# Performance work log

Measured on AMD Instinct MI355X. Metric: run time of the kernel, lower is better.

The kernel has to match this reference:

```python
import jax, jax.numpy as jnp
import numpy as np

N, E, G = 65536, 262144, 2048
DIN, H, F, L, P, TASK = 9, 300, 32, 5, 3, 1
DG = H + F + 1024 + 167  # 1523


def setup_inputs() -> dict:
    key = jax.random.key(0)
    ks = jax.random.split(key, 24)
    s = 0.02
    inp = {
        'x': jax.random.normal(ks[0], (N, DIN), jnp.float32),
        'morgan': jax.random.uniform(ks[1], (G, 1024), jnp.float32),
        'maccs': jax.random.uniform(ks[2], (G, 167), jnp.float32),
        'edge_index': jax.random.randint(ks[3], (2, E), 0, N, jnp.int32),
        'batch': jnp.sort(jax.random.randint(ks[4], (N,), 0, G, jnp.int32)),
        # node feature encoder
        'W_emb': s * jax.random.normal(ks[5], (DIN, H), jnp.float32),
        'b_emb': jnp.zeros((H,), jnp.float32),
        # GIN conv MLPs (L layers): H -> 2H -> H
        'gin_W1': s * jax.random.normal(ks[6], (L, H, 2 * H), jnp.float32),
        'gin_b1': jnp.zeros((L, 2 * H), jnp.float32),
        'gin_W2': s * jax.random.normal(ks[7], (L, 2 * H, H), jnp.float32),
        'gin_b2': jnp.zeros((L, H), jnp.float32),
        'bn_scale': jnp.ones((L, H), jnp.float32),
        'bn_bias': jnp.zeros((L, H), jnp.float32),
        'eps': jnp.zeros((L,), jnp.float32),
        # virtual node: init embedding + update MLPs (L-1 layers)
        'vn0': jnp.zeros((H,), jnp.float32),
        'vn_W1': s * jax.random.normal(ks[8], (L - 1, H, 2 * H), jnp.float32),
        'vn_b1': jnp.zeros((L - 1, 2 * H), jnp.float32),
        'vn_W2': s * jax.random.normal(ks[9], (L - 1, 2 * H, H), jnp.float32),
        'vn_b2': jnp.zeros((L - 1, H), jnp.float32),
        # predictor MLP: DG -> 2H -> TASK
        'Wp1': s * jax.random.normal(ks[10], (DG, 2 * H), jnp.float32),
        'bp1': jnp.zeros((2 * H,), jnp.float32),
        'Wp2': s * jax.random.normal(ks[11], (2 * H, TASK), jnp.float32),
        'bp2': jnp.zeros((TASK,), jnp.float32),
    }
    return inp


def _seg_mean(v, seg, n):
    s = jax.ops.segment_sum(v, seg, num_segments=n)
    c = jax.ops.segment_sum(jnp.ones((v.shape[0], 1), v.dtype), seg, num_segments=n)
    return s / jnp.maximum(c, 1.0)


def _bn(z, scale, bias):
    m = z.mean(0)
    v = z.var(0)
    return (z - m) * jax.lax.rsqrt(v + 1e-5) * scale + bias


def _gnn_and_predict(x, morgan, maccs, W_emb, b_emb, gin_W1, gin_b1, gin_W2, gin_b2,
                     bn_scale, bn_bias, eps, vn0, vn_W1, vn_b1, vn_W2, vn_b2,
                     Wp1, bp1, Wp2, bp2, edge_index, batch):
    n = x.shape[0]
    g = morgan.shape[0]
    nl = gin_W1.shape[0]
    src, dst = edge_index[0], edge_index[1]

    # GIN-virtual backbone (eval mode, dropout off). Note: GNN input is the
    # original x (the permuted ids are appended AFTER the GNN), so h is
    # permutation-independent and computed once.
    h = x @ W_emb + b_emb
    vn = jnp.broadcast_to(vn0, (g, vn0.shape[0]))
    for l in range(nl):
        hv = h + vn[batch]                                       # [N,H]
        agg = jax.ops.segment_sum(hv[src], dst, num_segments=n)  # neighbor sum
        z = (1.0 + eps[l]) * hv + agg
        z = jax.nn.relu(z @ gin_W1[l] + gin_b1[l]) @ gin_W2[l] + gin_b2[l]
        z = _bn(z, bn_scale[l], bn_bias[l])
        if l < nl - 1:
            z = jax.nn.relu(z)
        h = h + z  # residual
        if l < nl - 1:  # virtual node update
            vt = jax.ops.segment_sum(hv, batch, num_segments=g) + vn
            vn = vn + jax.nn.relu(jax.nn.relu(vt @ vn_W1[l] + vn_b1[l]) @ vn_W2[l] + vn_b2[l])

    pooled_h = _seg_mean(h, batch, g)  # [G,H]

    # Segmented random permutation of tiled eye(F) ids, averaged over P perms.
    # Each node gets one_hot(perm_rank_within_graph % F); rank computed by a
    # single lexsort over (batch, random) instead of a per-graph Python loop.
    counts = jax.ops.segment_sum(jnp.ones((n,), jnp.int32), batch, num_segments=g)
    starts = jnp.concatenate([jnp.zeros((1,), jnp.int32),
                              jnp.cumsum(counts)[:-1].astype(jnp.int32)])
    pkey = jax.random.key(42)
    acc = jnp.zeros((g, F), h.dtype)
    for p in range(P):
        r = jax.random.uniform(jax.random.fold_in(pkey, p), (n,))
        order = jnp.lexsort((r, batch))                       # sort by graph, then random
        local = jnp.arange(n, dtype=jnp.int32) - starts[batch[order]]
        rank = jnp.zeros((n,), jnp.int32).at[order].set(local)  # random rank in graph
        ids = jax.nn.one_hot(rank % F, F, dtype=h.dtype)        # [N,F]
        acc = acc + _seg_mean(ids, batch, g)
    id_pool = acc / P

    # h_rep order matches torch: [pooled h | pooled ids | morgan | maccs]
    h_rep = jnp.concatenate([pooled_h, id_pool, morgan, maccs], axis=1)  # [G,1523]
    return jax.nn.relu(h_rep @ Wp1 + bp1) @ Wp2 + bp2  # [G,TASK]


def reference(x, morgan, maccs, W_emb, b_emb, gin_W1, gin_b1, gin_W2, gin_b2,
              bn_scale, bn_bias, eps, vn0, vn_W1, vn_b1, vn_W2, vn_b2,
              Wp1, bp1, Wp2, bp2, edge_index, batch):
    return _gnn_and_predict(x, morgan, maccs, W_emb, b_emb, gin_W1, gin_b1,
                            gin_W2, gin_b2, bn_scale, bn_bias, eps, vn0,
                            vn_W1, vn_b1, vn_W2, vn_b2, Wp1, bp1, Wp2, bp2,
                            edge_index, batch)
```

## Files before the change

### kernel.cpp

```cpp
#include <hip/hip_runtime.h>

typedef unsigned short u16;
typedef unsigned int u32;
typedef __attribute__((ext_vector_type(8))) short bf16x8_t;
typedef __attribute__((ext_vector_type(4))) float f32x4_t;

#define kN 65536
#define kE 262144
#define kG 2048
#define kH 300
#define kH2 600
#define kL 5
#define kF 32
#define kDG 1523
#define KP_H 320
#define KP_H2 640
#define KP_DG 1536
#define NP_H2 640
#define NP_H 320
#define HVS 320
#define HVS32 160
#define WFRAG_PER_L 204800

__device__ __forceinline__ float bf2f(u16 x) {
    union { u32 u; float f; } v; v.u = ((u32)x) << 16; return v.f;
}
__device__ __forceinline__ u16 f2bf(float f) {
    union { float f; u32 u; } v; v.f = f;
    u32 u = v.u;
    u32 r = (u + 0x7fffu + ((u >> 16) & 1u)) >> 16;
    return (u16)r;
}
__device__ __forceinline__ float blo(u32 v) { return bf2f((u16)(v & 0xffffu)); }
__device__ __forceinline__ float bhi(u32 v) { return bf2f((u16)(v >> 16)); }
__device__ __forceinline__ u32 pack2(float lo, float hi) {
    return (u32)f2bf(lo) | ((u32)f2bf(hi) << 16);
}

__device__ __forceinline__ void gld16(const u16* g, u16* l) {
    __builtin_amdgcn_global_load_lds(
        (const __attribute__((address_space(1))) u32*)g,
        (__attribute__((address_space(3))) u32*)l, 16, 0, 0);
}

__device__ __forceinline__ void vwait6() { asm volatile("s_waitcnt vmcnt(6)" ::: "memory"); }
__device__ __forceinline__ void vwait8() { asm volatile("s_waitcnt vmcnt(8)" ::: "memory"); }
__device__ __forceinline__ void vwait0() { asm volatile("s_waitcnt vmcnt(0)" ::: "memory"); }
__device__ __forceinline__ void lwait0() { asm volatile("s_waitcnt lgkmcnt(0)" ::: "memory"); }
__device__ __forceinline__ void rbar() {
    __builtin_amdgcn_sched_barrier(0);
    __builtin_amdgcn_s_barrier();
    __builtin_amdgcn_sched_barrier(0);
}

__device__ __forceinline__ void swz_tile(int& m, int& n) {
    int p = blockIdx.x + gridDim.x * blockIdx.y;
    int xcd = p & 7;
    int q = p >> 3;
    int NB = gridDim.y;
    int mb8 = gridDim.x >> 3;
    m = xcd * mb8 + q / NB;
    n = q % NB;
}

__global__ void transpose_k(const float* __restrict__ W, u16* __restrict__ Wt,
                            int K, int NN, int NP, int KP, long total) {
    long idx = (long)blockIdx.x * 256 + threadIdx.x;
    if (idx >= total) return;
    int per = NP * KP;
    int b = (int)(idx / per);
    int r = (int)(idx % per);
    int n = r / KP;
    int k = r % KP;
    u16 v = 0;
    if (n < NN && k < K) v = f2bf(W[(long)b * K * NN + (long)k * NN + n]);
    Wt[idx] = v;
}

__global__ void pack_w1_k(const float* __restrict__ W, u16* __restrict__ Wf, long total) {
    long idx = (long)blockIdx.x * 256 + threadIdx.x;
    if (idx >= total) return;
    int l = (int)(idx / WFRAG_PER_L);
    long r = idx % WFRAG_PER_L;
    int e = (int)(r & 7);
    long r1 = r >> 3;
    int ln = (int)(r1 & 63);
    int l16 = ln & 15, quad = ln >> 4;
    long s = r1 >> 6;
    int tk = (int)(s % 10);
    long s2 = s / 10;
    int nt = (int)(s2 & 1);
    long s3 = s2 >> 1;
    int w = (int)(s3 & 3);
    int c = (int)(s3 >> 2);
    int n = c * 128 + w * 32 + nt * 16 + l16;
    int k = tk * 32 + quad * 8 + e;
    u16 v = 0;
    if (n < kH2 && k < kH) v = f2bf(W[(long)l * kH * kH2 + (long)k * kH2 + n]);
    Wf[idx] = v;
}

__global__ void pack_w2_k(const float* __restrict__ W, u16* __restrict__ Wf, long total) {
    long idx = (long)blockIdx.x * 256 + threadIdx.x;
    if (idx >= total) return;
    int l = (int)(idx / WFRAG_PER_L);
    long r = idx % WFRAG_PER_L;
    int e = (int)(r & 7);
    long r1 = r >> 3;
    int ln = (int)(r1 & 63);
    int l16 = ln & 15, quad = ln >> 4;
    long s = r1 >> 6;
    int ks = (int)(s & 3);
    long s2 = s >> 2;
    int nt = (int)(s2 % 5);
    long s3 = s2 / 5;
    int w = (int)(s3 & 3);
    int c = (int)(s3 >> 2);
    int n = w * 80 + nt * 16 + l16;
    int k = c * 128 + ks * 32 + quad * 8 + e;
    u16 v = 0;
    if (n < kH && k < kH2) v = f2bf(W[(long)l * kH2 * kH + (long)k * kH + n]);
    Wf[idx] = v;
}

__global__ void hist_g_k(const int* __restrict__ batch, int* __restrict__ counts) {
    int n = blockIdx.x * 256 + threadIdx.x;
    if (n < kN) atomicAdd(&counts[batch[n]], 1);
}

__global__ void scan_g_k(const int* __restrict__ counts, int* __restrict__ starts) {
    __shared__ int s[1024];
    int t = threadIdx.x;
    int c0 = counts[2 * t], c1 = counts[2 * t + 1];
    s[t] = c0 + c1;
    __syncthreads();
    for (int off = 1; off < 1024; off <<= 1) {
        int v = (t >= off) ? s[t - off] : 0;
        __syncthreads();
        s[t] += v;
        __syncthreads();
    }
    int excl = (t > 0) ? s[t - 1] : 0;
    starts[2 * t] = excl;
    starts[2 * t + 1] = excl + c0;
}

__global__ void hist_n_k(const int* __restrict__ ei, int* __restrict__ cnt) {
    int e = blockIdx.x * 256 + threadIdx.x;
    if (e < kE) atomicAdd(&cnt[ei[kE + e]], 1);
}

__global__ void scanA_k(const int* __restrict__ cnt, int* __restrict__ start, int* __restrict__ bsum) {
    __shared__ int s[1024];
    int b = blockIdx.x, t = threadIdx.x;
    int v = cnt[b * 1024 + t];
    s[t] = v;
    __syncthreads();
    for (int off = 1; off < 1024; off <<= 1) {
        int u = (t >= off) ? s[t - off] : 0;
        __syncthreads();
        s[t] += u;
        __syncthreads();
    }
    start[b * 1024 + t] = s[t] - v;
    if (t == 1023) bsum[b] = s[1023];
}

__global__ void scanB_k(int* __restrict__ bsum) {
    if (threadIdx.x == 0) {
        int s = 0;
        for (int i = 0; i < kN / 1024; i++) { s += bsum[i]; bsum[i] = s; }
    }
}

__global__ void scanC_k(int* __restrict__ start, const int* __restrict__ bsum) {
    int b = blockIdx.x, t = threadIdx.x;
    int add = (b > 0) ? bsum[b - 1] : 0;
    start[b * 1024 + t] += add;
    if (b == kN / 1024 - 1 && t == 1023) start[kN] = bsum[kN / 1024 - 1];
}

__global__ void fill_n_k(const int* __restrict__ ei, const int* __restrict__ start,
                         int* __restrict__ fill, int* __restrict__ perm) {
    int e = blockIdx.x * 256 + threadIdx.x;
    if (e >= kE) return;
    int s = ei[e], d = ei[kE + e];
    int pos = start[d] + atomicAdd(&fill[d], 1);
    perm[pos] = s;
}

__global__ __launch_bounds__(256) void embed_k(
    const float* __restrict__ x, const float* __restrict__ W,
    const float* __restrict__ b, const float* __restrict__ vn0,
    u32* __restrict__ hv32) {
    __shared__ float sW[9 * kH];
    __shared__ float sBV[kH];
    int tid = threadIdx.x;
    for (int i = tid; i < 9 * kH; i += 256) sW[i] = W[i];
    for (int i = tid; i < kH; i += 256) sBV[i] = b[i] + vn0[i];
    __syncthreads();
    int wave = tid >> 6, lane = tid & 63;
    int n = blockIdx.x * 4 + wave;
    float xv[9];
    #pragma unroll
    for (int d = 0; d < 9; d++) xv[d] = x[n * 9 + d];
    #pragma unroll
    for (int p = 0; p < 3; p++) {
        int ii = lane + p * 64;
        if (ii < 150) {
            int c0 = 2 * ii;
            float a0 = sBV[c0], a1 = sBV[c0 + 1];
            #pragma unroll
            for (int d = 0; d < 9; d++) {
                a0 += xv[d] * sW[d * kH + c0];
                a1 += xv[d] * sW[d * kH + c0 + 1];
            }
            hv32[(long)n * HVS32 + ii] = pack2(a0, a1);
        } else if (ii < HVS32) {
            hv32[(long)n * HVS32 + ii] = 0u;
        }
    }
}

__global__ void vninit_k(const float* __restrict__ vn0, float* __restrict__ vn) {
    int g = blockIdx.x, c = threadIdx.x;
    if (c < kH) vn[g * kH + c] = vn0[c];
}

__global__ __launch_bounds__(256) void gather_combine_k(
    const u32* __restrict__ hv32, const int* __restrict__ start_n,
    const int* __restrict__ perm, const float* __restrict__ eps, int l,
    u32* __restrict__ out32, float* __restrict__ stats) {
    int tid = threadIdx.x;
    int wave = tid >> 6, lane = tid & 63;
    int n = blockIdx.x * 4 + wave;
    int st = start_n[n], en = start_n[n + 1];
    int i0 = lane, i1 = lane + 64, i2 = lane + 128;
    bool p2 = (i2 < 150);
    float a0 = 0.f, b0 = 0.f, a1 = 0.f, b1 = 0.f, a2 = 0.f, b2 = 0.f;
    int e = st;
    for (; e + 4 <= en; e += 4) {
        const u32* rA = hv32 + (long)perm[e] * HVS32;
        const u32* rB = hv32 + (long)perm[e + 1] * HVS32;
        const u32* rC = hv32 + (long)perm[e + 2] * HVS32;
        const u32* rD = hv32 + (long)perm[e + 3] * HVS32;
        u32 vA0 = rA[i0], vA1 = rA[i1], vA2 = p2 ? rA[i2] : 0u;
        u32 vB0 = rB[i0], vB1 = rB[i1], vB2 = p2 ? rB[i2] : 0u;
        u32 vC0 = rC[i0], vC1 = rC[i1], vC2 = p2 ? rC[i2] : 0u;
        u32 vD0 = rD[i0], vD1 = rD[i1], vD2 = p2 ? rD[i2] : 0u;
        a0 += (blo(vA0) + blo(vB0)) + (blo(vC0) + blo(vD0));
        b0 += (bhi(vA0) + bhi(vB0)) + (bhi(vC0) + bhi(vD0));
        a1 += (blo(vA1) + blo(vB1)) + (blo(vC1) + blo(vD1));
        b1 += (bhi(vA1) + bhi(vB1)) + (bhi(vC1) + bhi(vD1));
        a2 += (blo(vA2) + blo(vB2)) + (blo(vC2) + blo(vD2));
        b2 += (bhi(vA2) + bhi(vB2)) + (bhi(vC2) + bhi(vD2));
    }
    for (; e + 2 <= en; e += 2) {
        const u32* rA = hv32 + (long)perm[e] * HVS32;
        const u32* rB = hv32 + (long)perm[e + 1] * HVS32;
        u32 vA0 = rA[i0], vA1 = rA[i1], vA2 = p2 ? rA[i2] : 0u;
        u32 vB0 = rB[i0], vB1 = rB[i1], vB2 = p2 ? rB[i2] : 0u;
        a0 += blo(vA0) + blo(vB0); b0 += bhi(vA0) + bhi(vB0);
        a1 += blo(vA1) + blo(vB1); b1 += bhi(vA1) + bhi(vB1);
        a2 += blo(vA2) + blo(vB2); b2 += bhi(vA2) + bhi(vB2);
    }
    if (e < en) {
        const u32* rA = hv32 + (long)perm[e] * HVS32;
        u32 vA0 = rA[i0], vA1 = rA[i1], vA2 = p2 ? rA[i2] : 0u;
        a0 += blo(vA0); b0 += bhi(vA0);
        a1 += blo(vA1); b1 += bhi(vA1);
        a2 += blo(vA2); b2 += bhi(vA2);
    }
    const u32* self = hv32 + (long)n * HVS32;
    float ep = 1.f + eps[l];
    u32 s0 = self[i0], s1 = self[i1];
    u32* o = out32 + (long)n * HVS32;
    o[i0] = pack2(ep * blo(s0) + a0, ep * bhi(s0) + b0);
    o[i1] = pack2(ep * blo(s1) + a1, ep * bhi(s1) + b1);
    if (p2) {
        u32 s2 = self[i2];
        o[i2] = pack2(ep * blo(s2) + a2, ep * bhi(s2) + b2);
    } else if (i2 < HVS32) {
        o[i2] = 0u;
    }
    int gz = blockIdx.x * 256 + tid;
    if (gz < 2 * kH) stats[gz] = 0.f;
}

__global__ __launch_bounds__(256) void vt_fin_k(
    const u32* __restrict__ hv32, const float* __restrict__ vncur,
    const int* __restrict__ counts, const int* __restrict__ starts,
    u32* __restrict__ vt32) {
    int tid = threadIdx.x, wave = tid >> 6, lane = tid & 63;
    int g = blockIdx.x * 4 + wave;
    int cnt = counts[g], st = starts[g];
    int i0 = lane, i1 = lane + 64, i2 = lane + 128;
    bool p2 = (i2 < 150);
    float a0 = 0.f, b0 = 0.f, a1 = 0.f, b1 = 0.f, a2 = 0.f, b2 = 0.f;
    int i = 0;
    for (; i + 4 <= cnt; i += 4) {
        const u32* rA = hv32 + (long)(st + i) * HVS32;
        const u32* rB = hv32 + (long)(st + i + 1) * HVS32;
        const u32* rC = hv32 + (long)(st + i + 2) * HVS32;
        const u32* rD = hv32 + (long)(st + i + 3) * HVS32;
        u32 vA0 = rA[i0], vA1 = rA[i1], vA2 = p2 ? rA[i2] : 0u;
        u32 vB0 = rB[i0], vB1 = rB[i1], vB2 = p2 ? rB[i2] : 0u;
        u32 vC0 = rC[i0], vC1 = rC[i1], vC2 = p2 ? rC[i2] : 0u;
        u32 vD0 = rD[i0], vD1 = rD[i1], vD2 = p2 ? rD[i2] : 0u;
        a0 += (blo(vA0) + blo(vB0)) + (blo(vC0) + blo(vD0));
        b0 += (bhi(vA0) + bhi(vB0)) + (bhi(vC0) + bhi(vD0));
        a1 += (blo(vA1) + blo(vB1)) + (blo(vC1) + blo(vD1));
        b1 += (bhi(vA1) + bhi(vB1)) + (bhi(vC1) + bhi(vD1));
        a2 += (blo(vA2) + blo(vB2)) + (blo(vC2) + blo(vD2));
        b2 += (bhi(vA2) + bhi(vB2)) + (bhi(vC2) + bhi(vD2));
    }
    for (; i < cnt; i++) {
        const u32* rA = hv32 + (long)(st + i) * HVS32;
        u32 vA0 = rA[i0], vA1 = rA[i1], vA2 = p2 ? rA[i2] : 0u;
        a0 += blo(vA0); b0 += bhi(vA0);
        a1 += blo(vA1); b1 += bhi(vA1);
        a2 += blo(vA2); b2 += bhi(vA2);
    }
    const float* vg = vncur + g * kH;
    vt32[(long)g * HVS32 + i0] = pack2(a0 + vg[2 * i0], b0 + vg[2 * i0 + 1]);
    vt32[(long)g * HVS32 + i1] = pack2(a1 + vg[2 * i1], b1 + vg[2 * i1 + 1]);
    if (p2) vt32[(long)g * HVS32 + i2] = pack2(a2 + vg[2 * i2], b2 + vg[2 * i2 + 1]);
    else if (i2 < HVS32) vt32[(long)g * HVS32 + i2] = 0u;
}

__global__ __launch_bounds__(256, 2) void fused_mlp_k(
    const u16* __restrict__ A,
    const u16* __restrict__ W1f,
    const float* __restrict__ b1,
    const u16* __restrict__ W2f,
    const float* __restrict__ b2,
    u16* __restrict__ outp,
    float* __restrict__ stats) {
    __shared__ __align__(16) u16 lA[5][64 * 64];
    __shared__ __align__(16) u16 z1c[2][64 * 128];
    __shared__ float sred[320][2];

    const int tid = threadIdx.x;
    const int lane = tid & 63;
    const int wave = tid >> 6;
    const int l16 = lane & 15;
    const int quad = lane >> 4;
    const long tm = (long)blockIdx.x * 64;
    const int srow = lane >> 3;
    const int sch = (lane & 7) ^ srow;

    for (int i = tid; i < 320; i += 256) { sred[i][0] = 0.f; sred[i][1] = 0.f; }

    #pragma unroll
    for (int t = 0; t < 5; t++) {
        #pragma unroll
        for (int j = 0; j < 2; j++) {
            int rb = wave * 16 + j * 8;
            gld16(A + (tm + rb + srow) * KP_H + t * 64 + sch * 8, &lA[t][rb * 64]);
        }
    }

    float rb1[5][2];
    #pragma unroll
    for (int c = 0; c < 5; c++)
        #pragma unroll
        for (int nt = 0; nt < 2; nt++) {
            int gc = c * 128 + wave * 32 + nt * 16 + l16;
            rb1[c][nt] = (gc < kH2) ? b1[gc] : 0.f;
        }
    float rb2[5];
    #pragma unroll
    for (int nt = 0; nt < 5; nt++) {
        int col = wave * 80 + nt * 16 + l16;
        rb2[nt] = (col < kH) ? b2[col] : 0.f;
    }

    f32x4_t acc2[4][5];
    #pragma unroll
    for (int i = 0; i < 4; i++)
        #pragma unroll
        for (int j = 0; j < 5; j++) acc2[i][j] = (f32x4_t){0.f, 0.f, 0.f, 0.f};

    vwait0();
    rbar();

    #pragma unroll
    for (int c = 0; c < 5; c++) {
        f32x4_t acc1[4][2];
        #pragma unroll
        for (int i = 0; i < 4; i++) {
            acc1[i][0] = (f32x4_t){0.f, 0.f, 0.f, 0.f};
            acc1[i][1] = (f32x4_t){0.f, 0.f, 0.f, 0.f};
        }
        const u16* w1p = W1f + ((long)((c * 4 + wave) * 2) * 10) * 512 + lane * 8;
        bf16x8_t wf[4][2];
        #pragma unroll
        for (int p = 0; p < 3; p++) {
            wf[p][0] = *(const bf16x8_t*)(w1p + p * 512);
            wf[p][1] = *(const bf16x8_t*)(w1p + 10 * 512 + p * 512);
        }
        #pragma unroll
        for (int tk = 0; tk < 10; tk++) {
            if (tk + 3 < 10) {
                wf[(tk + 3) & 3][0] = *(const bf16x8_t*)(w1p + (tk + 3) * 512);
                wf[(tk + 3) & 3][1] = *(const bf16x8_t*)(w1p + 10 * 512 + (tk + 3) * 512);
            }
            const int t = tk >> 1, ks = tk & 1;
            bf16x8_t af[4];
            #pragma unroll
            for (int mt = 0; mt < 4; mt++) {
                int row = mt * 16 + l16;
                int phys = (ks * 4 + quad) ^ (l16 & 7);
                af[mt] = *(const bf16x8_t*)&lA[t][row * 64 + phys * 8];
            }
            __builtin_amdgcn_s_setprio(1);
            #pragma unroll
            for (int mt = 0; mt < 4; mt++) {
                acc1[mt][0] = __builtin_amdgcn_mfma_f32_16x16x32_bf16(af[mt], wf[tk & 3][0], acc1[mt][0], 0, 0, 0);
                acc1[mt][1] = __builtin_amdgcn_mfma_f32_16x16x32_bf16(af[mt], wf[tk & 3][1], acc1[mt][1], 0, 0, 0);
            }
            __builtin_amdgcn_s_setprio(0);
        }

        const u16* w2p = W2f + ((long)((c * 4 + wave) * 5) * 4) * 512 + lane * 8;
        bf16x8_t wg[2][5];
        #pragma unroll
        for (int nt = 0; nt < 5; nt++) {
            wg[0][nt] = *(const bf16x8_t*)(w2p + nt * 4 * 512);
            wg[1][nt] = *(const bf16x8_t*)(w2p + nt * 4 * 512 + 512);
        }

        u16* zb = z1c[c & 1];
        #pragma unroll
        for (int nt = 0; nt < 2; nt++) {
            int col = wave * 32 + nt * 16 + l16;
            #pragma unroll
            for (int mt = 0; mt < 4; mt++) {
                #pragma unroll
                for (int r = 0; r < 4; r++) {
                    int row = mt * 16 + quad * 4 + r;
                    float v = fmaxf(acc1[mt][nt][r] + rb1[c][nt], 0.f);
                    int phys = (col >> 3) ^ (row & 15);
                    zb[row * 128 + phys * 8 + (col & 7)] = f2bf(v);
                }
            }
        }
        lwait0();
        rbar();

        #pragma unroll
        for (int ks = 0; ks < 4; ks++) {
            bf16x8_t af[4];
            #pragma unroll
            for (int mt = 0; mt < 4; mt++) {
                int row = mt * 16 + l16;
                int phys = (ks * 4 + quad) ^ (row & 15);
                af[mt] = *(const bf16x8_t*)&zb[row * 128 + phys * 8];
            }
            __builtin_amdgcn_s_setprio(1);
            #pragma unroll
            for (int mt = 0; mt < 4; mt++)
                #pragma unroll
                for (int nt = 0; nt < 5; nt++)
                    acc2[mt][nt] = __builtin_amdgcn_mfma_f32_16x16x32_bf16(af[mt], wg[ks & 1][nt], acc2[mt][nt], 0, 0, 0);
            __builtin_amdgcn_s_setprio(0);
            if (ks + 2 < 4) {
                #pragma unroll
                for (int nt = 0; nt < 5; nt++)
                    wg[ks & 1][nt] = *(const bf16x8_t*)(w2p + nt * 4 * 512 + (ks + 2) * 512);
            }
        }
    }

    #pragma unroll
    for (int nt = 0; nt < 5; nt++) {
        int col = wave * 80 + nt * 16 + l16;
        float s = 0.f, s2 = 0.f;
        #pragma unroll
        for (int mt = 0; mt < 4; mt++) {
            #pragma unroll
            for (int r = 0; r < 4; r++) {
                long row = tm + mt * 16 + quad * 4 + r;
                float v = acc2[mt][nt][r] + rb2[nt];
                float sv = (col < kH) ? v : 0.f;
                outp[row * KP_H + col] = f2bf(sv);
                s += sv; s2 += sv * sv;
            }
        }
        atomicAdd(&sred[col][0], s);
        atomicAdd(&sred[col][1], s2);
    }
    __syncthreads();
    for (int i = tid; i < kH; i += 256) {
        atomicAdd(&stats[i], sred[i][0]);
        atomicAdd(&stats[kH + i], sred[i][1]);
    }
}

template<int ACT, int OUT_BF16, int BN_STATS>
__global__ __launch_bounds__(256) void gemm_k(
    const u16* __restrict__ A, const u16* __restrict__ Wt,
    const float* __restrict__ bias, void* __restrict__ out,
    float* __restrict__ stats,
    int KP, int NN, int out_stride, int store_cols) {
    __shared__ __align__(16) u16 lA[2][128 * 64];
    __shared__ __align__(16) u16 lB[2][128 * 64];
    __shared__ float sred[128][2];

    const int tid = threadIdx.x;
    const int lane = tid & 63;
    const int wave = tid >> 6;
    const int l16 = lane & 15;
    const int quad = lane >> 4;
    const int wm = (wave & 1) * 64;
    const int wn = (wave >> 1) * 64;
    int sm, sn;
    swz_tile(sm, sn);
    const long tm = (long)sm * 128;
    const int tn = sn * 128;

    const int srow = lane >> 3;
    const int sch = (lane & 7) ^ srow;

    f32x4_t acc[4][4];
    #pragma unroll
    for (int i = 0; i < 4; i++)
        #pragma unroll
        for (int j = 0; j < 4; j++) acc[i][j] = (f32x4_t){0.f, 0.f, 0.f, 0.f};

    auto stage = [&](int bb, int k0) {
        #pragma unroll
        for (int j = 0; j < 4; j++) {
            int rb = wave * 32 + j * 8;
            int r = rb + srow;
            gld16(A + (tm + r) * KP + k0 + sch * 8, &lA[bb][rb * 64]);
            gld16(Wt + (long)(tn + r) * KP + k0 + sch * 8, &lB[bb][rb * 64]);
        }
    };

    const int nk = KP >> 6;
    stage(0, 0);
    if (nk > 1) stage(1, 64);
    for (int t = 0; t < nk; t++) {
        if (t < nk - 1) vwait8(); else vwait0();
        rbar();
        const u16* la = lA[t & 1];
        const u16* lb = lB[t & 1];
        #pragma unroll
        for (int ks = 0; ks < 2; ks++) {
            bf16x8_t af[4], bfr[4];
            #pragma unroll
            for (int mt = 0; mt < 4; mt++) {
                int row = wm + mt * 16 + l16;
                int phys = (ks * 4 + quad) ^ (l16 & 7);
                af[mt] = *(const bf16x8_t*)&la[row * 64 + phys * 8];
            }
            #pragma unroll
            for (int nt = 0; nt < 4; nt++) {
                int row = wn + nt * 16 + l16;
                int phys = (ks * 4 + quad) ^ (l16 & 7);
                bfr[nt] = *(const bf16x8_t*)&lb[row * 64 + phys * 8];
            }
            #pragma unroll
            for (int mt = 0; mt < 4; mt++)
                #pragma unroll
                for (int nt = 0; nt < 4; nt++)
                    acc[mt][nt] = __builtin_amdgcn_mfma_f32_16x16x32_bf16(af[mt], bfr[nt], acc[mt][nt], 0, 0, 0);
        }
        rbar();
        if (t + 2 < nk) stage(t & 1, (t + 2) * 64);
    }

    if (BN_STATS) {
        if (tid < 128) { sred[tid][0] = 0.f; sred[tid][1] = 0.f; }
    }
    __syncthreads();

    #pragma unroll
    for (int nt = 0; nt < 4; nt++) {
        int col = tn + wn + nt * 16 + l16;
        float bv = (col < NN) ? bias[col] : 0.f;
        float s = 0.f, s2 = 0.f;
        #pragma unroll
        for (int mt = 0; mt < 4; mt++) {
            #pragma unroll
            for (int r = 0; r < 4; r++) {
                long row = tm + wm + mt * 16 + quad * 4 + r;
                float v = acc[mt][nt][r] + bv;
                if (ACT) v = fmaxf(v, 0.f);
                float sv = (col < NN) ? v : 0.f;
                if (col < store_cols) {
                    if (OUT_BF16) ((u16*)out)[row * out_stride + col] = f2bf(sv);
                    else          ((float*)out)[row * out_stride + col] = sv;
                }
                s += sv; s2 += sv * sv;
            }
        }
        if (BN_STATS) {
            atomicAdd(&sred[wn + nt * 16 + l16][0], s);
            atomicAdd(&sred[wn + nt * 16 + l16][1], s2);
        }
    }
    if (BN_STATS) {
        __syncthreads();
        if (tid < 128) {
            int col = tn + tid;
            if (col < NN) {
                atomicAdd(&stats[col], sred[tid][0]);
                atomicAdd(&stats[NN + col], sred[tid][1]);
            }
        }
    }
}

template<int ACT, int OUT_MODE, int BN_STATS>
__global__ __launch_bounds__(256) void gemm64_k(
    const u16* __restrict__ A, const u16* __restrict__ Wt,
    const float* __restrict__ bias, void* __restrict__ out,
    float* __restrict__ stats, const float* __restrict__ vnacc,
    int KP, int NN, int out_stride, int store_cols) {
    __shared__ __align__(16) u16 lA[2][128 * 64];
    __shared__ __align__(16) u16 lB[2][64 * 64];
    __shared__ float sred[64][2];

    const int tid = threadIdx.x;
    const int lane = tid & 63;
    const int wave = tid >> 6;
    const int l16 = lane & 15;
    const int quad = lane >> 4;
    const int wm = (wave & 1) * 64;
    const int wn = (wave >> 1) * 32;
    int sm, sn;
    swz_tile(sm, sn);
    const long tm = (long)sm * 128;
    const int tn = sn * 64;

    const int srow = lane >> 3;
    const int sch = (lane & 7) ^ srow;

    f32x4_t acc[4][2];
    #pragma unroll
    for (int i = 0; i < 4; i++)
        #pragma unroll
        for (int j = 0; j < 2; j++) acc[i][j] = (f32x4_t){0.f, 0.f, 0.f, 0.f};

    auto stage = [&](int bb, int k0) {
        #pragma unroll
        for (int j = 0; j < 4; j++) {
            int rb = wave * 32 + j * 8;
            gld16(A + (tm + rb + srow) * KP + k0 + sch * 8, &lA[bb][rb * 64]);
        }
        #pragma unroll
        for (int j = 0; j < 2; j++) {
            int rb = wave * 16 + j * 8;
            gld16(Wt + (long)(tn + rb + srow) * KP + k0 + sch * 8, &lB[bb][rb * 64]);
        }
    };

    const int nk = KP >> 6;
    stage(0, 0);
    if (nk > 1) stage(1, 64);
    for (int t = 0; t < nk; t++) {
        if (t < nk - 1) vwait6(); else vwait0();
        rbar();
        const u16* la = lA[t & 1];
        const u16* lb = lB[t & 1];
        #pragma unroll
        for (int ks = 0; ks < 2; ks++) {
            bf16x8_t af[4], bfr[2];
            #pragma unroll
            for (int mt = 0; mt < 4; mt++) {
                int row = wm + mt * 16 + l16;
                int phys = (ks * 4 + quad) ^ (l16 & 7);
                af[mt] = *(const bf16x8_t*)&la[row * 64 + phys * 8];
            }
            #pragma unroll
            for (int nt = 0; nt < 2; nt++) {
                int row = wn + nt * 16 + l16;
                int phys = (ks * 4 + quad) ^ (l16 & 7);
                bfr[nt] = *(const bf16x8_t*)&lb[row * 64 + phys * 8];
            }
            #pragma unroll
            for (int mt = 0; mt < 4; mt++)
                #pragma unroll
                for (int nt = 0; nt < 2; nt++)
                    acc[mt][nt] = __builtin_amdgcn_mfma_f32_16x16x32_bf16(af[mt], bfr[nt], acc[mt][nt], 0, 0, 0);
        }
        rbar();
        if (t + 2 < nk) stage(t & 1, (t + 2) * 64);
    }

    if (BN_STATS) {
        if (tid < 64) { sred[tid][0] = 0.f; sred[tid][1] = 0.f; }
    }
    __syncthreads();

    #pragma unroll
    for (int nt = 0; nt < 2; nt++) {
        int col = tn + wn + nt * 16 + l16;
        float bv = (col < NN) ? bias[col] : 0.f;
        float s = 0.f, s2 = 0.f;
        #pragma unroll
        for (int mt = 0; mt < 4; mt++) {
            #pragma unroll
            for (int r = 0; r < 4; r++) {
                long row = tm + wm + mt * 16 + quad * 4 + r;
                float v = acc[mt][nt][r] + bv;
                if (ACT) v = fmaxf(v, 0.f);
                float sv = (col < NN) ? v : 0.f;
                if (col < store_cols) {
                    if (OUT_MODE == 1) ((u16*)out)[row * out_stride + col] = f2bf(sv);
                    else if (OUT_MODE == 2)
                        ((float*)out)[row * out_stride + col] =
                            vnacc[row * out_stride + col] + fmaxf(v, 0.f);
                    else ((float*)out)[row * out_stride + col] = sv;
                }
                s += sv; s2 += sv * sv;
            }
        }
        if (BN_STATS) {
            atomicAdd(&sred[wn + nt * 16 + l16][0], s);
            atomicAdd(&sred[wn + nt * 16 + l16][1], s2);
        }
    }
    if (BN_STATS) {
        __syncthreads();
        if (tid < 64) {
            int col = tn + tid;
            if (col < NN) {
                atomicAdd(&stats[col], sred[tid][0]);
                atomicAdd(&stats[NN + col], sred[tid][1]);
            }
        }
    }
}

template<int RELU>
__global__ __launch_bounds__(256) void resid_k(
    u32* __restrict__ hvb32, const u32* __restrict__ z32,
    const float* __restrict__ stats,
    const float* __restrict__ scale, const float* __restrict__ bias, int l,
    const int* __restrict__ batch,
    const float* __restrict__ vncur, const float* __restrict__ vnnxt) {
    int tid = threadIdx.x;
    int wave = tid >> 6, lane = tid & 63;
    int n = blockIdx.x * 4 + wave;
    int g = batch[n];
    #pragma unroll
    for (int p = 0; p < 3; p++) {
        int ii = lane + p * 64;
        if (ii >= 150) break;
        int c0 = 2 * ii;
        float m0 = stats[c0] * (1.f / (float)kN), m1 = stats[c0 + 1] * (1.f / (float)kN);
        float v0 = fmaxf(stats[kH + c0] * (1.f / (float)kN) - m0 * m0, 0.f);
        float v1 = fmaxf(stats[kH + c0 + 1] * (1.f / (float)kN) - m1 * m1, 0.f);
        float a0 = scale[l * kH + c0] * rsqrtf(v0 + 1e-5f);
        float a1 = scale[l * kH + c0 + 1] * rsqrtf(v1 + 1e-5f);
        float d0 = bias[l * kH + c0] - m0 * a0;
        float d1 = bias[l * kH + c0 + 1] - m1 * a1;
        u32 zz = z32[(long)n * HVS32 + ii];
        u32 ho = hvb32[(long)n * HVS32 + ii];
        float2 vc = *(const float2*)(vncur + g * kH + c0);
        float2 vx = *(const float2*)(vnnxt + g * kH + c0);
        float t0 = blo(zz) * a0 + d0;
        float t1 = bhi(zz) * a1 + d1;
        if (RELU) { t0 = fmaxf(t0, 0.f); t1 = fmaxf(t1, 0.f); }
        float h0 = (blo(ho) - vc.x) + t0;
        float h1 = (bhi(ho) - vc.y) + t1;
        hvb32[(long)n * HVS32 + ii] = pack2(h0 + vx.x, h1 + vx.y);
    }
}

__global__ __launch_bounds__(256) void pooled_k(
    const u32* __restrict__ hv32, const float* __restrict__ vnlast,
    const int* __restrict__ counts, const int* __restrict__ starts,
    u32* __restrict__ hrep32) {
    int tid = threadIdx.x, wave = tid >> 6, lane = tid & 63;
    int g = blockIdx.x * 4 + wave;
    int cnt = counts[g], st = starts[g];
    int i0 = lane, i1 = lane + 64, i2 = lane + 128;
    bool p2 = (i2 < 150);
    float a0 = 0.f, b0 = 0.f, a1 = 0.f, b1 = 0.f, a2 = 0.f, b2 = 0.f;
    int i = 0;
    for (; i + 4 <= cnt; i += 4) {
        const u32* rA = hv32 + (long)(st + i) * HVS32;
        const u32* rB = hv32 + (long)(st + i + 1) * HVS32;
        const u32* rC = hv32 + (long)(st + i + 2) * HVS32;
        const u32* rD = hv32 + (long)(st + i + 3) * HVS32;
        u32 vA0 = rA[i0], vA1 = rA[i1], vA2 = p2 ? rA[i2] : 0u;
        u32 vB0 = rB[i0], vB1 = rB[i1], vB2 = p2 ? rB[i2] : 0u;
        u32 vC0 = rC[i0], vC1 = rC[i1], vC2 = p2 ? rC[i2] : 0u;
        u32 vD0 = rD[i0], vD1 = rD[i1], vD2 = p2 ? rD[i2] : 0u;
        a0 += (blo(vA0) + blo(vB0)) + (blo(vC0) + blo(vD0));
        b0 += (bhi(vA0) + bhi(vB0)) + (bhi(vC0) + bhi(vD0));
        a1 += (blo(vA1) + blo(vB1)) + (blo(vC1) + blo(vD1));
        b1 += (bhi(vA1) + bhi(vB1)) + (bhi(vC1) + bhi(vD1));
        a2 += (blo(vA2) + blo(vB2)) + (blo(vC2) + blo(vD2));
        b2 += (bhi(vA2) + bhi(vB2)) + (bhi(vC2) + bhi(vD2));
    }
    for (; i < cnt; i++) {
        const u32* rA = hv32 + (long)(st + i) * HVS32;
        u32 vA0 = rA[i0], vA1 = rA[i1], vA2 = p2 ? rA[i2] : 0u;
        a0 += blo(vA0); b0 += bhi(vA0);
        a1 += blo(vA1); b1 += bhi(vA1);
        a2 += blo(vA2); b2 += bhi(vA2);
    }
    float fc = (float)cnt;
    float inv = 1.f / (float)(cnt > 0 ? cnt : 1);
    const float* vg = vnlast + g * kH;
    hrep32[(long)g * 768 + i0] = pack2((a0 - fc * vg[2 * i0]) * inv, (b0 - fc * vg[2 * i0 + 1]) * inv);
    hrep32[(long)g * 768 + i1] = pack2((a1 - fc * vg[2 * i1]) * inv, (b1 - fc * vg[2 * i1 + 1]) * inv);
    if (p2)
        hrep32[(long)g * 768 + i2] = pack2((a2 - fc * vg[2 * i2]) * inv, (b2 - fc * vg[2 * i2 + 1]) * inv);
}

__global__ void hrep_rest_k(const float* __restrict__ morgan, const float* __restrict__ maccs,
                            const int* __restrict__ counts, u16* __restrict__ hrep) {
    long idx = (long)blockIdx.x * 256 + threadIdx.x;
    if (idx >= (long)kG * (KP_DG - kH)) return;
    int g = (int)(idx / (KP_DG - kH));
    int j = (int)(idx % (KP_DG - kH));
    int col = kH + j;
    u16 v;
    if (j < kF) {
        int c = counts[g];
        int q = (j < c) ? ((c - 1 - j) / kF + 1) : 0;
        v = f2bf((float)q / (float)(c > 0 ? c : 1));
    } else if (j < kF + 1024) {
        v = f2bf(morgan[(long)g * 1024 + (j - kF)]);
    } else if (j < kF + 1024 + 167) {
        v = f2bf(maccs[(long)g * 167 + (j - kF - 1024)]);
    } else {
        v = 0;
    }
    hrep[(long)g * KP_DG + col] = v;
}

__global__ void final_k(const u16* __restrict__ zp, const float* __restrict__ Wp2,
                        const float* __restrict__ bp2, float* __restrict__ out) {
    int wave = threadIdx.x >> 6, lane = threadIdx.x & 63;
    int g = blockIdx.x * 4 + wave;
    float acc = 0.f;
    for (int c = lane; c < kH2; c += 64) acc += bf2f(zp[(long)g * KP_H2 + c]) * Wp2[c];
    #pragma unroll
    for (int off = 32; off; off >>= 1) acc += __shfl_down(acc, off);
    if (lane == 0) out[g] = acc + bp2[0];
}

extern "C" void kernel_launch(void* const* d_in, const int* in_sizes, int n_in,
                              void* d_out, int out_size, void* d_ws, size_t ws_size,
                              hipStream_t stream) {
    const float* x      = (const float*)d_in[0];
    const float* morgan = (const float*)d_in[1];
    const float* maccs  = (const float*)d_in[2];
    const int*   ei     = (const int*)d_in[3];
    const int*   batch  = (const int*)d_in[4];
    const float* W_emb  = (const float*)d_in[5];
    const float* b_emb  = (const float*)d_in[6];
    const float* gin_W1 = (const float*)d_in[7];
    const float* gin_b1 = (const float*)d_in[8];
    const float* gin_W2 = (const float*)d_in[9];
    const float* gin_b2 = (const float*)d_in[10];
    const float* bn_scale = (const float*)d_in[11];
    const float* bn_bias  = (const float*)d_in[12];
    const float* eps    = (const float*)d_in[13];
    const float* vn0    = (const float*)d_in[14];
    const float* vn_W1  = (const float*)d_in[15];
    const float* vn_b1  = (const float*)d_in[16];
    const float* vn_W2  = (const float*)d_in[17];
    const float* vn_b2  = (const float*)d_in[18];
    const float* Wp1    = (const float*)d_in[19];
    const float* bp1    = (const float*)d_in[20];
    const float* Wp2    = (const float*)d_in[21];
    const float* bp2    = (const float*)d_in[22];
    float* out = (float*)d_out;

    char* ws = (char*)d_ws;
    size_t off = 0;
    auto alloc = [&](size_t bytes) -> char* {
        char* p = ws + off;
        off += (bytes + 255) & ~(size_t)255;
        return p;
    };
    u16*   hvbf = (u16*)alloc((size_t)kN * HVS * 2);
    u16*   hv   = (u16*)alloc((size_t)kN * KP_H * 2);
    u16*   z1   = (u16*)alloc((size_t)kN * KP_H2 * 2);
    float* vnA  = (float*)alloc((size_t)kG * kH * 4);
    float* vnB  = (float*)alloc((size_t)kG * kH * 4);
    int* counts = (int*)alloc(kG * 4);
    int* starts = (int*)alloc(kG * 4);
    float* stats = (float*)alloc(2 * kH * 4);
    int* cnt_n  = (int*)alloc((size_t)kN * 4);
    int* start_n = (int*)alloc((size_t)(kN + 1) * 4);
    int* fill_n = (int*)alloc((size_t)kN * 4);
    int* bsum   = (int*)alloc((kN / 1024) * 4);
    int* perm   = (int*)alloc((size_t)kE * 4);
    u16* W1f   = (u16*)alloc((size_t)kL * WFRAG_PER_L * 2);
    u16* W2f   = (u16*)alloc((size_t)kL * WFRAG_PER_L * 2);
    u16* Wt_v1 = (u16*)alloc((size_t)(kL - 1) * NP_H2 * KP_H * 2);
    u16* Wt_v2 = (u16*)alloc((size_t)(kL - 1) * NP_H * KP_H2 * 2);
    u16* Wt_p1 = (u16*)alloc((size_t)NP_H2 * KP_DG * 2);
    if (off > ws_size) return;

    u16* vt_in = z1;
    u16* z1v   = z1 + (size_t)4 * 1024 * 1024;
    u16* hrep  = z1;
    u16* zp    = z1 + (size_t)8 * 1024 * 1024;
    float* vnb[2] = {vnA, vnB};

    {
        long tf = (long)kL * WFRAG_PER_L;
        pack_w1_k<<<dim3((unsigned)((tf + 255) / 256)), 256, 0, stream>>>(gin_W1, W1f, tf);
        pack_w2_k<<<dim3((unsigned)((tf + 255) / 256)), 256, 0, stream>>>(gin_W2, W2f, tf);
        long t3 = (long)(kL - 1) * NP_H2 * KP_H;
        transpose_k<<<dim3((unsigned)((t3 + 255) / 256)), 256, 0, stream>>>(vn_W1, Wt_v1, kH, kH2, NP_H2, KP_H, t3);
        long t4 = (long)(kL - 1) * NP_H * KP_H2;
        transpose_k<<<dim3((unsigned)((t4 + 255) / 256)), 256, 0, stream>>>(vn_W2, Wt_v2, kH2, kH, NP_H, KP_H2, t4);
        long t5 = (long)NP_H2 * KP_DG;
        transpose_k<<<dim3((unsigned)((t5 + 255) / 256)), 256, 0, stream>>>(Wp1, Wt_p1, kDG, kH2, NP_H2, KP_DG, t5);
    }

    hipMemsetAsync(counts, 0, kG * 4, stream);
    hipMemsetAsync(cnt_n, 0, (size_t)kN * 4, stream);
    hipMemsetAsync(fill_n, 0, (size_t)kN * 4, stream);
    hist_g_k<<<kN / 256, 256, 0, stream>>>(batch, counts);
    scan_g_k<<<1, 1024, 0, stream>>>(counts, starts);
    hist_n_k<<<kE / 256, 256, 0, stream>>>(ei, cnt_n);
    scanA_k<<<kN / 1024, 1024, 0, stream>>>(cnt_n, start_n, bsum);
    scanB_k<<<1, 64, 0, stream>>>(bsum);
    scanC_k<<<kN / 1024, 1024, 0, stream>>>(start_n, bsum);
    fill_n_k<<<kE / 256, 256, 0, stream>>>(ei, start_n, fill_n, perm);

    embed_k<<<kN / 4, 256, 0, stream>>>(x, W_emb, b_emb, vn0, (u32*)hvbf);
    vninit_k<<<kG, 320, 0, stream>>>(vn0, vnA);

    for (int l = 0; l < kL; l++) {
        float* vcur = vnb[l & 1];
        float* vnxt = vnb[(l + 1) & 1];
        gather_combine_k<<<kN / 4, 256, 0, stream>>>(
            (const u32*)hvbf, start_n, perm, eps, l, (u32*)hv, stats);
        if (l < kL - 1) {
            vt_fin_k<<<kG / 4, 256, 0, stream>>>(
                (const u32*)hvbf, vcur, counts, starts, (u32*)vt_in);
            gemm_k<1, 1, 0><<<dim3(16, NP_H2 / 128), 256, 0, stream>>>(
                vt_in, Wt_v1 + (size_t)l * NP_H2 * KP_H, vn_b1 + l * kH2,
                z1v, nullptr, KP_H, kH2, KP_H2, KP_H2);
            gemm64_k<0, 2, 0><<<dim3(16, NP_H / 64), 256, 0, stream>>>(
                z1v, Wt_v2 + (size_t)l * NP_H * KP_H2, vn_b2 + l * kH,
                vnxt, nullptr, vcur, KP_H2, kH, kH, kH);
        }
        fused_mlp_k<<<kN / 64, 256, 0, stream>>>(
            hv, W1f + (size_t)l * WFRAG_PER_L, gin_b1 + l * kH2,
            W2f + (size_t)l * WFRAG_PER_L, gin_b2 + l * kH,
            hv, stats);
        if (l < kL - 1)
            resid_k<1><<<kN / 4, 256, 0, stream>>>(
                (u32*)hvbf, (const u32*)hv, stats, bn_scale, bn_bias, l, batch, vcur, vnxt);
        else
            resid_k<0><<<kN / 4, 256, 0, stream>>>(
                (u32*)hvbf, (const u32*)hv, stats, bn_scale, bn_bias, l, batch, vcur, vcur);
    }

    float* vnlast = vnb[(kL - 1) & 1];
    pooled_k<<<kG / 4, 256, 0, stream>>>(
        (const u32*)hvbf, vnlast, counts, starts, (u32*)hrep);
    {
        long tr = (long)kG * (KP_DG - kH);
        hrep_rest_k<<<dim3((unsigned)((tr + 255) / 256)), 256, 0, stream>>>(morgan, maccs, counts, hrep);
    }
    gemm_k<1, 1, 0><<<dim3(16, NP_H2 / 128), 256, 0, stream>>>(
        hrep, Wt_p1, bp1, zp, nullptr, KP_DG, kH2, KP_H2, KP_H2);
    final_k<<<kG / 4, 256, 0, stream>>>(zp, Wp2, bp2, out);
}
```

Before: 1.151 ms.

## Fuse virtual-node two-layer MLP into single kernel with packed weight fragments

Replaces the two separate GEMM launches for the virtual-node MLP (H->2H with ReLU, then 2H->H plus residual) with one fused kernel. The kernel keeps each 64-row block's hidden activations in shared memory and reads pre-packed MFMA weight fragments, the same layout the GIN MLP kernel uses. This removes the global round trip of the 2048x640 intermediate and one launch per layer. In exchange the grid is small: only 32 blocks, each of which streams all weights, so occupancy for this step drops.

Result: no change. 1.128 ms (-1.9%).

```diff
diff --git a/kernel.cpp b/kernel.cpp
--- a/kernel.cpp
+++ b/kernel.cpp
@@ -43,7 +43,6 @@
         (__attribute__((address_space(3))) u32*)l, 16, 0, 0);
 }
 
-__device__ __forceinline__ void vwait6() { asm volatile("s_waitcnt vmcnt(6)" ::: "memory"); }
 __device__ __forceinline__ void vwait8() { asm volatile("s_waitcnt vmcnt(8)" ::: "memory"); }
 __device__ __forceinline__ void vwait0() { asm volatile("s_waitcnt vmcnt(0)" ::: "memory"); }
 __device__ __forceinline__ void lwait0() { asm volatile("s_waitcnt lgkmcnt(0)" ::: "memory"); }
@@ -497,6 +496,164 @@
     }
 }
 
+__global__ __launch_bounds__(256, 2) void fused_vn_k(
+    const u16* __restrict__ A,
+    const u16* __restrict__ W1f,
+    const float* __restrict__ b1,
+    const u16* __restrict__ W2f,
+    const float* __restrict__ b2,
+    const float* __restrict__ vncur,
+    float* __restrict__ vnnxt) {
+    __shared__ __align__(16) u16 lA[5][64 * 64];
+    __shared__ __align__(16) u16 z1c[2][64 * 128];
+
+    const int tid = threadIdx.x;
+    const int lane = tid & 63;
+    const int wave = tid >> 6;
+    const int l16 = lane & 15;
+    const int quad = lane >> 4;
+    const long tm = (long)blockIdx.x * 64;
+    const int srow = lane >> 3;
+    const int sch = (lane & 7) ^ srow;
+
+    #pragma unroll
+    for (int t = 0; t < 5; t++) {
+        #pragma unroll
+        for (int j = 0; j < 2; j++) {
+            int rb = wave * 16 + j * 8;
+            gld16(A + (tm + rb + srow) * KP_H + t * 64 + sch * 8, &lA[t][rb * 64]);
+        }
+    }
+
+    float rb1[5][2];
+    #pragma unroll
+    for (int c = 0; c < 5; c++)
+        #pragma unroll
+        for (int nt = 0; nt < 2; nt++) {
+            int gc = c * 128 + wave * 32 + nt * 16 + l16;
+            rb1[c][nt] = (gc < kH2) ? b1[gc] : 0.f;
+        }
+    float rb2[5];
+    #pragma unroll
+    for (int nt = 0; nt < 5; nt++) {
+        int col = wave * 80 + nt * 16 + l16;
+        rb2[nt] = (col < kH) ? b2[col] : 0.f;
+    }
+
+    f32x4_t acc2[4][5];
+    #pragma unroll
+    for (int i = 0; i < 4; i++)
+        #pragma unroll
+        for (int j = 0; j < 5; j++) acc2[i][j] = (f32x4_t){0.f, 0.f, 0.f, 0.f};
+
+    vwait0();
+    rbar();
+
+    #pragma unroll
+    for (int c = 0; c < 5; c++) {
+        f32x4_t acc1[4][2];
+        #pragma unroll
+        for (int i = 0; i < 4; i++) {
+            acc1[i][0] = (f32x4_t){0.f, 0.f, 0.f, 0.f};
+            acc1[i][1] = (f32x4_t){0.f, 0.f, 0.f, 0.f};
+        }
+        const u16* w1p = W1f + ((long)((c * 4 + wave) * 2) * 10) * 512 + lane * 8;
+        bf16x8_t wf[4][2];
+        #pragma unroll
+        for (int p = 0; p < 3; p++) {
+            wf[p][0] = *(const bf16x8_t*)(w1p + p * 512);
+            wf[p][1] = *(const bf16x8_t*)(w1p + 10 * 512 + p * 512);
+        }
+        #pragma unroll
+        for (int tk = 0; tk < 10; tk++) {
+            if (tk + 3 < 10) {
+                wf[(tk + 3) & 3][0] = *(const bf16x8_t*)(w1p + (tk + 3) * 512);
+                wf[(tk + 3) & 3][1] = *(const bf16x8_t*)(w1p + 10 * 512 + (tk + 3) * 512);
+            }
+            const int t = tk >> 1, ks = tk & 1;
+            bf16x8_t af[4];
+            #pragma unroll
+            for (int mt = 0; mt < 4; mt++) {
+                int row = mt * 16 + l16;
+                int phys = (ks * 4 + quad) ^ (l16 & 7);
+                af[mt] = *(const bf16x8_t*)&lA[t][row * 64 + phys * 8];
+            }
+            __builtin_amdgcn_s_setprio(1);
+            #pragma unroll
+            for (int mt = 0; mt < 4; mt++) {
+                acc1[mt][0] = __builtin_amdgcn_mfma_f32_16x16x32_bf16(af[mt], wf[tk & 3][0], acc1[mt][0], 0, 0, 0);
+                acc1[mt][1] = __builtin_amdgcn_mfma_f32_16x16x32_bf16(af[mt], wf[tk & 3][1], acc1[mt][1], 0, 0, 0);
+            }
+            __builtin_amdgcn_s_setprio(0);
+        }
+
+        const u16* w2p = W2f + ((long)((c * 4 + wave) * 5) * 4) * 512 + lane * 8;
+        bf16x8_t wg[2][5];
+        #pragma unroll
+        for (int nt = 0; nt < 5; nt++) {
+            wg[0][nt] = *(const bf16x8_t*)(w2p + nt * 4 * 512);
+            wg[1][nt] = *(const bf16x8_t*)(w2p + nt * 4 * 512 + 512);
+        }
+
+        u16* zb = z1c[c & 1];
+        #pragma unroll
+        for (int nt = 0; nt < 2; nt++) {
+            int col = wave * 32 + nt * 16 + l16;
+            #pragma unroll
+            for (int mt = 0; mt < 4; mt++) {
+                #pragma unroll
+                for (int r = 0; r < 4; r++) {
+                    int row = mt * 16 + quad * 4 + r;
+                    float v = fmaxf(acc1[mt][nt][r] + rb1[c][nt], 0.f);
+                    int phys = (col >> 3) ^ (row & 15);
+                    zb[row * 128 + phys * 8 + (col & 7)] = f2bf(v);
+                }
+            }
+        }
+        lwait0();
+        rbar();
+
+        #pragma unroll
+        for (int ks = 0; ks < 4; ks++) {
+            bf16x8_t af[4];
+            #pragma unroll
+            for (int mt = 0; mt < 4; mt++) {
+                int row = mt * 16 + l16;
+                int phys = (ks * 4 + quad) ^ (row & 15);
+                af[mt] = *(const bf16x8_t*)&zb[row * 128 + phys * 8];
+            }
+            __builtin_amdgcn_s_setprio(1);
+            #pragma unroll
+            for (int mt = 0; mt < 4; mt++)
+                #pragma unroll
+                for (int nt = 0; nt < 5; nt++)
+                    acc2[mt][nt] = __builtin_amdgcn_mfma_f32_16x16x32_bf16(af[mt], wg[ks & 1][nt], acc2[mt][nt], 0, 0, 0);
+            __builtin_amdgcn_s_setprio(0);
+            if (ks + 2 < 4) {
+                #pragma unroll
+                for (int nt = 0; nt < 5; nt++)
+                    wg[ks & 1][nt] = *(const bf16x8_t*)(w2p + nt * 4 * 512 + (ks + 2) * 512);
+            }
+        }
+    }
+
+    #pragma unroll
+    for (int nt = 0; nt < 5; nt++) {
+        int col = wave * 80 + nt * 16 + l16;
+        if (col < kH) {
+            #pragma unroll
+            for (int mt = 0; mt < 4; mt++) {
+                #pragma unroll
+                for (int r = 0; r < 4; r++) {
+                    long row = tm + mt * 16 + quad * 4 + r;
+                    float v = fmaxf(acc2[mt][nt][r] + rb2[nt], 0.f);
+                    vnnxt[row * kH + col] = vncur[row * kH + col] + v;
+                }
+            }
+        }
+    }
+}
+
 template<int ACT, int OUT_BF16, int BN_STATS>
 __global__ __launch_bounds__(256) void gemm_k(
     const u16* __restrict__ A, const u16* __restrict__ Wt,
@@ -604,128 +761,6 @@
     if (BN_STATS) {
         __syncthreads();
         if (tid < 128) {
-            int col = tn + tid;
-            if (col < NN) {
-                atomicAdd(&stats[col], sred[tid][0]);
-                atomicAdd(&stats[NN + col], sred[tid][1]);
-            }
-        }
-    }
-}
-
-template<int ACT, int OUT_MODE, int BN_STATS>
-__global__ __launch_bounds__(256) void gemm64_k(
-    const u16* __restrict__ A, const u16* __restrict__ Wt,
-    const float* __restrict__ bias, void* __restrict__ out,
-    float* __restrict__ stats, const float* __restrict__ vnacc,
-    int KP, int NN, int out_stride, int store_cols) {
-    __shared__ __align__(16) u16 lA[2][128 * 64];
-    __shared__ __align__(16) u16 lB[2][64 * 64];
-    __shared__ float sred[64][2];
-
-    const int tid = threadIdx.x;
-    const int lane = tid & 63;
-    const int wave = tid >> 6;
-    const int l16 = lane & 15;
-    const int quad = lane >> 4;
-    const int wm = (wave & 1) * 64;
-    const int wn = (wave >> 1) * 32;
-    int sm, sn;
-    swz_tile(sm, sn);
-    const long tm = (long)sm * 128;
-    const int tn = sn * 64;
-
-    const int srow = lane >> 3;
-    const int sch = (lane & 7) ^ srow;
-
-    f32x4_t acc[4][2];
-    #pragma unroll
-    for (int i = 0; i < 4; i++)
-        #pragma unroll
-        for (int j = 0; j < 2; j++) acc[i][j] = (f32x4_t){0.f, 0.f, 0.f, 0.f};
-
-    auto stage = [&](int bb, int k0) {
-        #pragma unroll
-        for (int j = 0; j < 4; j++) {
-            int rb = wave * 32 + j * 8;
-            gld16(A + (tm + rb + srow) * KP + k0 + sch * 8, &lA[bb][rb * 64]);
-        }
-        #pragma unroll
-        for (int j = 0; j < 2; j++) {
-            int rb = wave * 16 + j * 8;
-            gld16(Wt + (long)(tn + rb + srow) * KP + k0 + sch * 8, &lB[bb][rb * 64]);
-        }
-    };
-
-    const int nk = KP >> 6;
-    stage(0, 0);
-    if (nk > 1) stage(1, 64);
-    for (int t = 0; t < nk; t++) {
-        if (t < nk - 1) vwait6(); else vwait0();
-        rbar();
-        const u16* la = lA[t & 1];
-        const u16* lb = lB[t & 1];
-        #pragma unroll
-        for (int ks = 0; ks < 2; ks++) {
-            bf16x8_t af[4], bfr[2];
-            #pragma unroll
-            for (int mt = 0; mt < 4; mt++) {
-                int row = wm + mt * 16 + l16;
-                int phys = (ks * 4 + quad) ^ (l16 & 7);
-                af[mt] = *(const bf16x8_t*)&la[row * 64 + phys * 8];
-            }
-            #pragma unroll
-            for (int nt = 0; nt < 2; nt++) {
-                int row = wn + nt * 16 + l16;
-                int phys = (ks * 4 + quad) ^ (l16 & 7);
-                bfr[nt] = *(const bf16x8_t*)&lb[row * 64 + phys * 8];
-            }
-            #pragma unroll
-            for (int mt = 0; mt < 4; mt++)
-                #pragma unroll
-                for (int nt = 0; nt < 2; nt++)
-                    acc[mt][nt] = __builtin_amdgcn_mfma_f32_16x16x32_bf16(af[mt], bfr[nt], acc[mt][nt], 0, 0, 0);
-        }
-        rbar();
-        if (t + 2 < nk) stage(t & 1, (t + 2) * 64);
-    }
-
-    if (BN_STATS) {
-        if (tid < 64) { sred[tid][0] = 0.f; sred[tid][1] = 0.f; }
-    }
-    __syncthreads();
-
-    #pragma unroll
-    for (int nt = 0; nt < 2; nt++) {
-        int col = tn + wn + nt * 16 + l16;
-        float bv = (col < NN) ? bias[col] : 0.f;
-        float s = 0.f, s2 = 0.f;
-        #pragma unroll
-        for (int mt = 0; mt < 4; mt++) {
-            #pragma unroll
-            for (int r = 0; r < 4; r++) {
-                long row = tm + wm + mt * 16 + quad * 4 + r;
-                float v = acc[mt][nt][r] + bv;
-                if (ACT) v = fmaxf(v, 0.f);
-                float sv = (col < NN) ? v : 0.f;
-                if (col < store_cols) {
-                    if (OUT_MODE == 1) ((u16*)out)[row * out_stride + col] = f2bf(sv);
-                    else if (OUT_MODE == 2)
-                        ((float*)out)[row * out_stride + col] =
-                            vnacc[row * out_stride + col] + fmaxf(v, 0.f);
-                    else ((float*)out)[row * out_stride + col] = sv;
-                }
-                s += sv; s2 += sv * sv;
-            }
-        }
-        if (BN_STATS) {
-            atomicAdd(&sred[wn + nt * 16 + l16][0], s);
-            atomicAdd(&sred[wn + nt * 16 + l16][1], s2);
-        }
-    }
-    if (BN_STATS) {
-        __syncthreads();
-        if (tid < 64) {
             int col = tn + tid;
             if (col < NN) {
                 atomicAdd(&stats[col], sred[tid][0]);
@@ -897,13 +932,12 @@
     int* perm   = (int*)alloc((size_t)kE * 4);
     u16* W1f   = (u16*)alloc((size_t)kL * WFRAG_PER_L * 2);
     u16* W2f   = (u16*)alloc((size_t)kL * WFRAG_PER_L * 2);
-    u16* Wt_v1 = (u16*)alloc((size_t)(kL - 1) * NP_H2 * KP_H * 2);
-    u16* Wt_v2 = (u16*)alloc((size_t)(kL - 1) * NP_H * KP_H2 * 2);
+    u16* Wv1f  = (u16*)alloc((size_t)(kL - 1) * WFRAG_PER_L * 2);
+    u16* Wv2f  = (u16*)alloc((size_t)(kL - 1) * WFRAG_PER_L * 2);
     u16* Wt_p1 = (u16*)alloc((size_t)NP_H2 * KP_DG * 2);
     if (off > ws_size) return;
 
     u16* vt_in = z1;
-    u16* z1v   = z1 + (size_t)4 * 1024 * 1024;
     u16* hrep  = z1;
     u16* zp    = z1 + (size_t)8 * 1024 * 1024;
     float* vnb[2] = {vnA, vnB};
@@ -912,10 +946,9 @@
         long tf = (long)kL * WFRAG_PER_L;
         pack_w1_k<<<dim3((unsigned)((tf + 255) / 256)), 256, 0, stream>>>(gin_W1, W1f, tf);
         pack_w2_k<<<dim3((unsigned)((tf + 255) / 256)), 256, 0, stream>>>(gin_W2, W2f, tf);
-        long t3 = (long)(kL - 1) * NP_H2 * KP_H;
-        transpose_k<<<dim3((unsigned)((t3 + 255) / 256)), 256, 0, stream>>>(vn_W1, Wt_v1, kH, kH2, NP_H2, KP_H, t3);
-        long t4 = (long)(kL - 1) * NP_H * KP_H2;
-        transpose_k<<<dim3((unsigned)((t4 + 255) / 256)), 256, 0, stream>>>(vn_W2, Wt_v2, kH2, kH, NP_H, KP_H2, t4);
+        long tv = (long)(kL - 1) * WFRAG_PER_L;
+        pack_w1_k<<<dim3((unsigned)((tv + 255) / 256)), 256, 0, stream>>>(vn_W1, Wv1f, tv);
+        pack_w2_k<<<dim3((unsigned)((tv + 255) / 256)), 256, 0, stream>>>(vn_W2, Wv2f, tv);
         long t5 = (long)NP_H2 * KP_DG;
         transpose_k<<<dim3((unsigned)((t5 + 255) / 256)), 256, 0, stream>>>(Wp1, Wt_p1, kDG, kH2, NP_H2, KP_DG, t5);
     }
@@ -942,12 +975,10 @@
         if (l < kL - 1) {
             vt_fin_k<<<kG / 4, 256, 0, stream>>>(
                 (const u32*)hvbf, vcur, counts, starts, (u32*)vt_in);
-            gemm_k<1, 1, 0><<<dim3(16, NP_H2 / 128), 256, 0, stream>>>(
-                vt_in, Wt_v1 + (size_t)l * NP_H2 * KP_H, vn_b1 + l * kH2,
-                z1v, nullptr, KP_H, kH2, KP_H2, KP_H2);
-            gemm64_k<0, 2, 0><<<dim3(16, NP_H / 64), 256, 0, stream>>>(
-                z1v, Wt_v2 + (size_t)l * NP_H * KP_H2, vn_b2 + l * kH,
-                vnxt, nullptr, vcur, KP_H2, kH, kH, kH);
+            fused_vn_k<<<kG / 64, 256, 0, stream>>>(
+                vt_in, Wv1f + (size_t)l * WFRAG_PER_L, vn_b1 + l * kH2,
+                Wv2f + (size_t)l * WFRAG_PER_L, vn_b2 + l * kH,
+                vcur, vnxt);
         }
         fused_mlp_k<<<kN / 64, 256, 0, stream>>>(
             hv, W1f + (size_t)l * WFRAG_PER_L, gin_b1 + l * kH2,
```
